# Kernel optimization log

Hardware: AMD Instinct MI355X
Metric: run time of the kernel (lower is better)

Reference implementation:

```python
import jax, jax.numpy as jnp
import numpy as np
import math

D = 2048          # embedding_size
H = 16            # nheads
HD = D // H       # head_dim
S = 2048          # seq_len
B = 2
# SwiGLU hidden per source: int(2*(4*D)/3) rounded up to multiple of 256
FF = 256 * ((int(2 * (4 * D) / 3) + 255) // 256)  # 5632
EPS = 1e-6


def pe_row(seq_len, d_model):
    # PositionalEncoding buffer, but forward uses only pe[:, seq_len-1]
    pos = float(seq_len - 1)
    div = jnp.exp(jnp.arange(0, d_model, 2, dtype=jnp.float32) * (-math.log(10000.0) / d_model))
    row = jnp.zeros((d_model,), jnp.float32)
    row = row.at[0::2].set(jnp.sin(pos * div))
    row = row.at[1::2].set(jnp.cos(pos * div))
    return row  # [D]


def rmsnorm(x, g, eps=EPS):
    xf = x.astype(jnp.float32)
    n = xf * jax.lax.rsqrt(jnp.mean(xf * xf, axis=-1, keepdims=True) + eps)
    return g * n.astype(x.dtype)


def setup_inputs() -> dict:
    key = jax.random.key(0)
    ks = jax.random.split(key, 16)
    sd = 0.02
    x = jax.random.normal(ks[0], (B, S, D), jnp.float32)
    mask = jnp.triu(jnp.ones((S, S), jnp.int32), k=1)[None, None]  # [1,1,S,S], 1 = masked
    return {
        'x': x,
        'mask': mask,
        'qkv_w': jax.random.normal(ks[1], (3 * D, D), jnp.float32) * sd,
        'qkv_b': jnp.zeros((3 * D,), jnp.float32),
        'fc_w': jax.random.normal(ks[2], (D, D), jnp.float32) * sd,
        'fc_b': jnp.zeros((D,), jnp.float32),
        'w1': jax.random.normal(ks[3], (FF, D), jnp.float32) * sd,
        'b1': jnp.zeros((FF,), jnp.float32),
        'w2': jax.random.normal(ks[4], (FF, D), jnp.float32) * sd,
        'b2': jnp.zeros((FF,), jnp.float32),
        'w3': jax.random.normal(ks[5], (D, FF), jnp.float32) * sd,
        'b3': jnp.zeros((D,), jnp.float32),
        'g_attn': jnp.ones((D,), jnp.float32),
        'g_ff': jnp.ones((D,), jnp.float32),
    }


def _block(x, mask, qkv_w, qkv_b, fc_w, fc_b, w1, b1, w2, b2, w3, b3, g_attn, g_ff):
    b, s, _ = x.shape
    # attention sublayer (pre-norm)
    h_in = rmsnorm(x, g_attn)
    qkv = h_in @ qkv_w.T + qkv_b
    xq, xk, xv = jnp.split(qkv, 3, axis=-1)
    pe = pe_row(s, D)  # single row added everywhere (faithful to source)
    xq = xq + pe
    xk = xk + pe
    q = xq.reshape(b, s, H, HD).transpose(0, 2, 1, 3)
    k = xk.reshape(b, s, H, HD).transpose(0, 2, 1, 3)
    v = xv.reshape(b, s, H, HD).transpose(0, 2, 1, 3)
    scores = jnp.einsum('bhqd,bhkd->bhqk', q, k) / math.sqrt(HD)
    scores = jnp.where(mask == 1, jnp.float32(-1e9), scores)
    attn = jax.nn.softmax(scores, axis=-1)
    out = jnp.einsum('bhqk,bhkd->bhqd', attn, v)
    out = out.transpose(0, 2, 1, 3).reshape(b, s, D)
    attn_out = out @ fc_w.T + fc_b
    h = x + attn_out
    # SwiGLU FFN sublayer (pre-norm)
    f_in = rmsnorm(h, g_ff)
    gate = jax.nn.silu(f_in @ w1.T + b1) * (f_in @ w2.T + b2)
    return h + gate @ w3.T + b3


def reference(x, mask, qkv_w, qkv_b, fc_w, fc_b, w1, b1, w2, b2, w3, b3, g_attn, g_ff):
    return _block(x, mask, qkv_w, qkv_b, fc_w, fc_b, w1, b1, w2, b2, w3, b3, g_attn, g_ff)
```

## Files before the change

kernel.cpp:

```cpp
#include <hip/hip_runtime.h>
#include <math.h>


typedef __attribute__((ext_vector_type(8))) short bf16x8;
typedef __attribute__((ext_vector_type(4))) short bf16x4;
typedef __attribute__((ext_vector_type(4))) float f32x4;

#define DEVI __device__ __forceinline__

DEVI unsigned short f2bf(float f) {
  unsigned u = __builtin_bit_cast(unsigned, f);
  u += 0x7FFFu + ((u >> 16) & 1u);
  return (unsigned short)(u >> 16);
}
DEVI float bf2f(unsigned short h) {
  unsigned u = ((unsigned)h) << 16;
  return __builtin_bit_cast(float, u);
}

#define GLL16(g, l) __builtin_amdgcn_global_load_lds( \
    (const __attribute__((address_space(1))) unsigned int*)(const void*)(g), \
    (__attribute__((address_space(3))) unsigned int*)(void*)(l), 16, 0, 0)

__global__ __launch_bounds__(256) void wconv_k(const float* __restrict__ src,
                                               unsigned short* __restrict__ dst,
                                               long n8) {
  long t = (long)blockIdx.x * 256 + threadIdx.x;
  if (t >= n8) return;
  const f32x4* s = (const f32x4*)(src + t * 8);
  f32x4 a = s[0], b = s[1];
  bf16x8 o;
#pragma unroll
  for (int j = 0; j < 4; ++j) {
    o[j]     = (short)f2bf(a[j]);
    o[4 + j] = (short)f2bf(b[j]);
  }
  *(bf16x8*)(dst + t * 8) = o;
}

__global__ void pe_k(float* __restrict__ pe) {
  int c = blockIdx.x * 256 + threadIdx.x;
  if (c >= 2048) return;
  int i2 = c & ~1;
  float div = __expf(-(float)i2 * (9.210340371976184f / 2048.0f));
  float ang = 2047.0f * div;
  pe[c] = (c & 1) ? cosf(ang) : sinf(ang);
}

__global__ __launch_bounds__(256) void rmsnorm_k(const float* __restrict__ x,
                                                 const float* __restrict__ g,
                                                 unsigned short* __restrict__ out) {
  long row = blockIdx.x;
  const float* xr = x + row * 2048;
  int tid = threadIdx.x;
  f32x4 v0 = *(const f32x4*)&xr[tid * 8];
  f32x4 v1 = *(const f32x4*)&xr[tid * 8 + 4];
  float ss = 0.f;
#pragma unroll
  for (int j = 0; j < 4; ++j) ss += v0[j] * v0[j] + v1[j] * v1[j];
#pragma unroll
  for (int m = 1; m < 64; m <<= 1) ss += __shfl_xor(ss, m, 64);
  __shared__ float red[4];
  int lane = tid & 63, wv = tid >> 6;
  if (lane == 0) red[wv] = ss;
  __syncthreads();
  float tot = red[0] + red[1] + red[2] + red[3];
  float rn = rsqrtf(tot * (1.0f / 2048.0f) + 1e-6f);
  const float* gr = g + tid * 8;
  bf16x8 o;
#pragma unroll
  for (int j = 0; j < 4; ++j) {
    o[j]     = (short)f2bf(v0[j] * rn * gr[j]);
    o[4 + j] = (short)f2bf(v1[j] * rn * gr[4 + j]);
  }
  *(bf16x8*)&out[row * 2048 + tid * 8] = o;
}

template <int EPI>
__global__ __launch_bounds__(512, 1) void gemm256(const unsigned short* __restrict__ A,
                                                  const unsigned short* __restrict__ W,
                                                  const float* __restrict__ bias,
                                                  const float* __restrict__ resid,
                                                  void* __restrict__ outv,
                                                  int M, int N, int K, int nbx) {
  __shared__ __align__(16) unsigned short Ab[3][256 * 64];
  __shared__ __align__(16) unsigned short Bb[3][128 * 64];
  const int tid  = threadIdx.x;
  const int lane = tid & 63;
  const int wv   = tid >> 6;
  const int wm   = wv >> 1;
  const int wn   = wv & 1;
  const int l15  = lane & 15;
  const int lg   = lane >> 4;
  const int cpx = gridDim.x >> 3;
  const int wg  = (blockIdx.x & 7) * cpx + (blockIdx.x >> 3);
  const long tm = (long)(wg / nbx) * 256;
  const long tn = (long)(wg % nbx) * 128;

  const int srow = wv * 8 + (lane >> 3);
  const int scol = (((lane & 7) ^ (lane >> 3)) << 3);
  const unsigned short* gA = A + (tm + srow) * (long)K + scol;
  const unsigned short* gB = W + (tn + srow) * (long)K + scol;

  const int KT = K >> 6;

#define STGA(buf, kt, g) GLL16(gA + ((long)(g) * 64) * K + ((long)(kt) << 6), \
                               &Ab[buf][(g) * 4096 + wv * 512])
#define STGB(buf, kt, g) GLL16(gB + ((long)(g) * 64) * K + ((long)(kt) << 6), \
                               &Bb[buf][(g) * 4096 + wv * 512])

  f32x4 acc[4][4] = {};

  STGA(0, 0, 0); STGA(0, 0, 1); STGA(0, 0, 2); STGA(0, 0, 3);
  STGB(0, 0, 0); STGB(0, 0, 1);
  STGA(1, 1, 0); STGA(1, 1, 1); STGA(1, 1, 2); STGA(1, 1, 3);
  STGB(1, 1, 0); STGB(1, 1, 1);
  asm volatile("s_waitcnt vmcnt(6)" ::: "memory");
  __builtin_amdgcn_s_barrier();

  int ct = 0;
  for (int t = 0; t < KT; ++t) {
    const int pt = (ct >= 1) ? (ct - 1) : 2;
    const bool pre = (t + 2) < KT;
    const unsigned short* At = &Ab[ct][0];
    const unsigned short* Bt = &Bb[ct][0];
#pragma unroll
    for (int kk = 0; kk < 2; ++kk) {
      bf16x8 af[4], bfv[4];
#pragma unroll
      for (int m = 0; m < 4; ++m)
        af[m] = *(const bf16x8*)&At[((wm * 64 + m * 16 + l15) * 8 +
                                     ((kk * 4 + lg) ^ (l15 & 7))) * 8];
#pragma unroll
      for (int n = 0; n < 4; ++n)
        bfv[n] = *(const bf16x8*)&Bt[((wn * 64 + n * 16 + l15) * 8 +
                                      ((kk * 4 + lg) ^ (l15 & 7))) * 8];
      if (pre) {
        if (kk == 0) { STGA(pt, t + 2, 0); STGA(pt, t + 2, 1); STGA(pt, t + 2, 2); }
        else         { STGA(pt, t + 2, 3); STGB(pt, t + 2, 0); STGB(pt, t + 2, 1); }
      }
      __builtin_amdgcn_s_barrier();
      __builtin_amdgcn_s_setprio(1);
#pragma unroll
      for (int m = 0; m < 4; ++m)
#pragma unroll
        for (int n = 0; n < 4; ++n)
          acc[m][n] = __builtin_amdgcn_mfma_f32_16x16x32_bf16(af[m], bfv[n], acc[m][n], 0, 0, 0);
      __builtin_amdgcn_s_setprio(0);
      if (kk == 0) {
        __builtin_amdgcn_s_barrier();
      } else {
        if (t + 2 < KT)      asm volatile("s_waitcnt vmcnt(6)" ::: "memory");
        else if (t + 1 < KT) asm volatile("s_waitcnt vmcnt(0)" ::: "memory");
        __builtin_amdgcn_s_barrier();
      }
    }
    ct = (ct + 1 >= 3) ? 0 : (ct + 1);
  }
#undef STGA
#undef STGB
  __builtin_amdgcn_sched_barrier(0);

  const long row0 = tm + wm * 64 + (lg << 2);
  const long col0 = tn + wn * 64;
#pragma unroll
  for (int n = 0; n < 4; ++n) {
    const long col = col0 + n * 16 + l15;
    const float bv = bias[col];
#pragma unroll
    for (int m = 0; m < 4; ++m) {
      const long rw = row0 + m * 16;
#pragma unroll
      for (int j = 0; j < 4; ++j) {
        const float v = acc[m][n][j] + bv;
        if (EPI == 0) {
          ((unsigned short*)outv)[(rw + j) * (long)N + col] = f2bf(v);
        } else {
          float* of = (float*)outv;
          const long i = (rw + j) * (long)N + col;
          of[i] = resid[i] + v;
        }
      }
    }
  }
}

__global__ __launch_bounds__(256) void krepack_k(const unsigned short* __restrict__ qkv,
                                                 const float* __restrict__ pe,
                                                 unsigned short* __restrict__ kpe) {
  long t = (long)blockIdx.x * 256 + threadIdx.x;
  long idx = t * 8;
  long row = idx >> 11;
  int cd  = (int)(idx & 2047);
  int h = cd >> 7, d = cd & 127;
  long b = row >> 11, s = row & 2047;
  bf16x8 v = *(const bf16x8*)&qkv[row * 6144 + 2048 + cd];
  const float* per = &pe[cd];
#pragma unroll
  for (int j = 0; j < 8; ++j)
    v[j] = (short)f2bf(bf2f((unsigned short)v[j]) + per[j]);
  *(bf16x8*)&kpe[(((b * 16 + h)) * 2048 + s) * 128 + d] = v;
}

__global__ __launch_bounds__(256) void vtrans_k(const unsigned short* __restrict__ qkv,
                                                unsigned short* __restrict__ Vt) {
  const int s0 = blockIdx.x * 64;
  const int d0 = blockIdx.y * 64;
  const int bh = blockIdx.z;
  const long b = bh >> 4;
  const int h = bh & 15;
  __shared__ unsigned short tile[64][76];
  const int t = threadIdx.x;
#pragma unroll
  for (int half = 0; half < 2; ++half) {
    int c = t + half * 256;
    int r = c >> 3;
    int cc = (c & 7) * 8;
    bf16x8 v = *(const bf16x8*)&qkv[(b * 2048 + s0 + r) * 6144 + 4096 + h * 128 + d0 + cc];
#pragma unroll
    for (int j = 0; j < 8; ++j) tile[cc + j][r] = (unsigned short)v[j];
  }
  __syncthreads();
#pragma unroll
  for (int half = 0; half < 2; ++half) {
    int c = t + half * 256;
    int dr = c >> 3;
    int sc = (c & 7) * 8;
    bf16x4 lo = *(const bf16x4*)&tile[dr][sc];
    bf16x4 hi = *(const bf16x4*)&tile[dr][sc + 4];
    bf16x8 v;
#pragma unroll
    for (int j = 0; j < 4; ++j) { v[j] = lo[j]; v[4 + j] = hi[j]; }
    *(bf16x8*)&Vt[((long)bh * 128 + d0 + dr) * 2048 + s0 + sc] = v;
  }
}

__global__ __launch_bounds__(256, 2) void fattn_k(const unsigned short* __restrict__ QKV,
                                                  const float* __restrict__ pe,
                                                  const unsigned short* __restrict__ Kp,
                                                  const unsigned short* __restrict__ Vt,
                                                  unsigned short* __restrict__ O) {
  const int lin = blockIdx.x;
  const int chunk = lin & 7;
  const int idx = lin >> 3;
  const int bh = chunk * 4 + (idx >> 4);
  const int i16 = idx & 15;
  const int qb = (i16 & 1) ? ((i16 - 1) >> 1) : (15 - (i16 >> 1));
  const long b = bh >> 4;
  const int h = bh & 15;
  const int q0 = qb * 128;
  const int tid = threadIdx.x, lane = tid & 63, wv = tid >> 6;
  const int l15 = lane & 15, lg = lane >> 4;
  const int qw = q0 + wv * 32;

  __shared__ __align__(16) unsigned short Kl[2][8192];
  __shared__ __align__(16) unsigned short Vl[2][8192];
  __shared__ __align__(16) unsigned short Plds[4][32][40];

  const float scale = 0.08838834764831845f;
  const unsigned short* Qb = QKV + (b * 2048 + qw) * 6144 + h * 128;
  bf16x8 qf[2][4];
#pragma unroll
  for (int r = 0; r < 2; ++r)
#pragma unroll
    for (int kc = 0; kc < 4; ++kc) {
      bf16x8 v = *(const bf16x8*)&Qb[(r * 16 + l15) * 6144 + kc * 32 + lg * 8];
      const float* per = &pe[h * 128 + kc * 32 + lg * 8];
#pragma unroll
      for (int j = 0; j < 8; ++j)
        v[j] = (short)f2bf((bf2f((unsigned short)v[j]) + per[j]) * scale);
      qf[r][kc] = v;
    }

  const unsigned short* Kg = Kp + (long)bh * 2048 * 128;
  const unsigned short* Vg = Vt + (long)bh * 128 * 2048;

  auto stage = [&](int buf, int key0) {
#pragma unroll
    for (int ld = 0; ld < 4; ++ld) {
      int sr = wv * 16 + ld * 4 + (lane >> 4);
      int sc = ((lane & 15) << 3) ^ ((sr & 7) << 3);
      GLL16(Kg + (long)(key0 + sr) * 128 + sc, &Kl[buf][wv * 2048 + ld * 512]);
      int dr = wv * 32 + ld * 8 + (lane >> 3);
      int dc = ((lane & 7) << 3) ^ ((dr & 7) << 3);
      GLL16(Vg + (long)dr * 2048 + key0 + dc, &Vl[buf][wv * 2048 + ld * 512]);
    }
  };

  f32x4 o[2][8] = {};
  float mr[2][4], sdn[2][4];
#pragma unroll
  for (int r = 0; r < 2; ++r)
#pragma unroll
    for (int j = 0; j < 4; ++j) { mr[r][j] = -1e30f; sdn[r][j] = 0.f; }

  const int nkt = (q0 >> 6) + 2;
  stage(0, 0);
  __syncthreads();
  int cur = 0;
  for (int kt = 0; kt < nkt; ++kt) {
    const int key0 = kt << 6;
    if (kt + 1 < nkt) stage(cur ^ 1, key0 + 64);
    if (key0 <= qw + 31) {
      f32x4 s[2][4] = {};
      __builtin_amdgcn_s_setprio(1);
#pragma unroll
      for (int ks = 0; ks < 4; ++ks) {
        bf16x8 kf[4];
#pragma unroll
        for (int kc = 0; kc < 4; ++kc)
          kf[kc] = *(const bf16x8*)&Kl[cur][(ks * 16 + l15) * 128 +
                                           ((kc * 32 + lg * 8) ^ ((l15 & 7) << 3))];
#pragma unroll
        for (int r = 0; r < 2; ++r)
#pragma unroll
          for (int kc = 0; kc < 4; ++kc)
            s[r][ks] = __builtin_amdgcn_mfma_f32_16x16x32_bf16(qf[r][kc], kf[kc], s[r][ks], 0, 0, 0);
      }
      __builtin_amdgcn_s_setprio(0);
      const bool maskt = (key0 + 63 > qw);
      float pm[2][4];
#pragma unroll
      for (int r = 0; r < 2; ++r)
#pragma unroll
        for (int j = 0; j < 4; ++j) pm[r][j] = -1e30f;
#pragma unroll
      for (int r = 0; r < 2; ++r)
#pragma unroll
        for (int ks = 0; ks < 4; ++ks)
#pragma unroll
          for (int j = 0; j < 4; ++j) {
            float v = s[r][ks][j];
            if (maskt) {
              int qrow = qw + r * 16 + lg * 4 + j;
              int key  = key0 + ks * 16 + l15;
              v = (key <= qrow) ? v : -1e30f;
              s[r][ks][j] = v;
            }
            pm[r][j] = fmaxf(pm[r][j], v);
          }
#pragma unroll
      for (int msk = 1; msk < 16; msk <<= 1)
#pragma unroll
        for (int r = 0; r < 2; ++r)
#pragma unroll
          for (int j = 0; j < 4; ++j) pm[r][j] = fmaxf(pm[r][j], __shfl_xor(pm[r][j], msk, 64));
      bool grow = false;
#pragma unroll
      for (int r = 0; r < 2; ++r)
#pragma unroll
        for (int j = 0; j < 4; ++j) grow = grow || (pm[r][j] > mr[r][j] + 8.0f);
      if (__any(grow)) {
#pragma unroll
        for (int r = 0; r < 2; ++r)
#pragma unroll
          for (int j = 0; j < 4; ++j) {
            float mn = fmaxf(mr[r][j], pm[r][j]);
            float corr = __expf(mr[r][j] - mn);
            mr[r][j] = mn;
            sdn[r][j] *= corr;
#pragma unroll
            for (int nf = 0; nf < 8; ++nf) o[r][nf][j] *= corr;
          }
      }
      float ps[2][4];
#pragma unroll
      for (int r = 0; r < 2; ++r)
#pragma unroll
        for (int j = 0; j < 4; ++j) ps[r][j] = 0.f;
#pragma unroll
      for (int r = 0; r < 2; ++r)
#pragma unroll
        for (int ks = 0; ks < 4; ++ks)
#pragma unroll
          for (int j = 0; j < 4; ++j) {
            float e = __expf(s[r][ks][j] - mr[r][j]);
            s[r][ks][j] = e;
            ps[r][j] += e;
          }
#pragma unroll
      for (int msk = 1; msk < 16; msk <<= 1)
#pragma unroll
        for (int r = 0; r < 2; ++r)
#pragma unroll
          for (int j = 0; j < 4; ++j) ps[r][j] += __shfl_xor(ps[r][j], msk, 64);
#pragma unroll
      for (int r = 0; r < 2; ++r)
#pragma unroll
        for (int j = 0; j < 4; ++j) sdn[r][j] += ps[r][j];
#pragma unroll
      for (int hk = 0; hk < 2; ++hk) {
#pragma unroll
        for (int r = 0; r < 2; ++r)
#pragma unroll
          for (int ks2 = 0; ks2 < 2; ++ks2)
#pragma unroll
            for (int j = 0; j < 4; ++j)
              Plds[wv][r * 16 + lg * 4 + j][ks2 * 16 + l15] = f2bf(s[r][hk * 2 + ks2][j]);
        bf16x8 pf[2];
#pragma unroll
        for (int r = 0; r < 2; ++r) {
          bf16x4 lo = *(const bf16x4*)&Plds[wv][r * 16 + l15][lg * 8];
          bf16x4 hi = *(const bf16x4*)&Plds[wv][r * 16 + l15][lg * 8 + 4];
          bf16x8 p;
#pragma unroll
          for (int j = 0; j < 4; ++j) { p[j] = lo[j]; p[4 + j] = hi[j]; }
          pf[r] = p;
        }
        __builtin_amdgcn_s_setprio(1);
#pragma unroll
        for (int nf = 0; nf < 8; ++nf) {
          bf16x8 vf = *(const bf16x8*)&Vl[cur][(nf * 16 + l15) * 64 +
                                              ((hk * 32 + lg * 8) ^ ((l15 & 7) << 3))];
#pragma unroll
          for (int r = 0; r < 2; ++r)
            o[r][nf] = __builtin_amdgcn_mfma_f32_16x16x32_bf16(pf[r], vf, o[r][nf], 0, 0, 0);
        }
        __builtin_amdgcn_s_setprio(0);
      }
    }
    __syncthreads();
    cur ^= 1;
  }
  unsigned short* Ob = O + (b * 2048 + qw) * 2048 + h * 128;
#pragma unroll
  for (int r = 0; r < 2; ++r)
#pragma unroll
    for (int j = 0; j < 4; ++j) {
      float inv = 1.0f / sdn[r][j];
#pragma unroll
      for (int nf = 0; nf < 8; ++nf)
        Ob[(long)(r * 16 + lg * 4 + j) * 2048 + nf * 16 + l15] = f2bf(o[r][nf][j] * inv);
    }
}

__global__ __launch_bounds__(256) void gate_k(const unsigned short* __restrict__ a1,
                                              const unsigned short* __restrict__ a2,
                                              unsigned short* __restrict__ g) {
  long idx = ((long)blockIdx.x * 256 + threadIdx.x) * 8;
  bf16x8 x1 = *(const bf16x8*)&a1[idx];
  bf16x8 x2 = *(const bf16x8*)&a2[idx];
  bf16x8 r;
#pragma unroll
  for (int j = 0; j < 8; ++j) {
    float f1 = bf2f((unsigned short)x1[j]);
    float f2v = bf2f((unsigned short)x2[j]);
    float sg = f1 / (1.0f + __expf(-f1));
    r[j] = (short)f2bf(sg * f2v);
  }
  *(bf16x8*)&g[idx] = r;
}

extern "C" void kernel_launch(void* const* d_in, const int* in_sizes, int n_in,
                              void* d_out, int out_size, void* d_ws, size_t ws_size,
                              hipStream_t stream) {
  (void)in_sizes; (void)n_in; (void)out_size; (void)ws_size;
  const float* x    = (const float*)d_in[0];
  const float* qkvw = (const float*)d_in[2];
  const float* qkvb = (const float*)d_in[3];
  const float* fcw  = (const float*)d_in[4];
  const float* fcb  = (const float*)d_in[5];
  const float* w1   = (const float*)d_in[6];
  const float* b1   = (const float*)d_in[7];
  const float* w2   = (const float*)d_in[8];
  const float* b2   = (const float*)d_in[9];
  const float* w3   = (const float*)d_in[10];
  const float* b3   = (const float*)d_in[11];
  const float* ga   = (const float*)d_in[12];
  const float* gf   = (const float*)d_in[13];

  char* ws = (char*)d_ws;
  size_t off = 0;
  auto alloc = [&](size_t bytes) -> char* {
    char* p = ws + off;
    off = (off + bytes + 255) & ~(size_t)255;
    return p;
  };
  unsigned short* wqkv  = (unsigned short*)alloc(6144L * 2048 * 2);
  unsigned short* wfc   = (unsigned short*)alloc(2048L * 2048 * 2);
  unsigned short* w1b   = (unsigned short*)alloc(5632L * 2048 * 2);
  unsigned short* w2b   = (unsigned short*)alloc(5632L * 2048 * 2);
  unsigned short* w3b   = (unsigned short*)alloc(2048L * 5632 * 2);
  float*          pe    = (float*)alloc(2048 * 4);
  unsigned short* hin   = (unsigned short*)alloc(4096L * 2048 * 2);
  unsigned short* qkv   = (unsigned short*)alloc(4096L * 6144 * 2);
  unsigned short* kpe   = (unsigned short*)alloc(4096L * 2048 * 2);
  unsigned short* Vt    = (unsigned short*)alloc(4096L * 2048 * 2);
  unsigned short* attnb = (unsigned short*)alloc(4096L * 2048 * 2);
  float* h = (float*)d_out;

  wconv_k<<<6144, 256, 0, stream>>>(qkvw, wqkv, 6144L * 2048 / 8);
  wconv_k<<<2048, 256, 0, stream>>>(fcw,  wfc,  2048L * 2048 / 8);
  wconv_k<<<5632, 256, 0, stream>>>(w1,   w1b,  5632L * 2048 / 8);
  wconv_k<<<5632, 256, 0, stream>>>(w2,   w2b,  5632L * 2048 / 8);
  wconv_k<<<5632, 256, 0, stream>>>(w3,   w3b,  2048L * 5632 / 8);
  pe_k<<<8, 256, 0, stream>>>(pe);

  rmsnorm_k<<<4096, 256, 0, stream>>>(x, ga, hin);
  gemm256<0><<<768, 512, 0, stream>>>(hin, wqkv, qkvb, nullptr, qkv, 4096, 6144, 2048, 48);
  krepack_k<<<4096, 256, 0, stream>>>(qkv, pe, kpe);
  vtrans_k<<<dim3(32, 2, 32), 256, 0, stream>>>(qkv, Vt);
  fattn_k<<<dim3(512), 256, 0, stream>>>(qkv, pe, kpe, Vt, attnb);
  gemm256<1><<<256, 512, 0, stream>>>(attnb, wfc, fcb, x, h, 4096, 2048, 2048, 16);

  rmsnorm_k<<<4096, 256, 0, stream>>>(h, gf, hin);
  unsigned short* a1 = qkv;
  unsigned short* a2 = kpe;
  gemm256<0><<<704, 512, 0, stream>>>(hin, w1b, b1, nullptr, a1, 4096, 5632, 2048, 44);
  gemm256<0><<<704, 512, 0, stream>>>(hin, w2b, b2, nullptr, a2, 4096, 5632, 2048, 44);
  gate_k<<<11264, 256, 0, stream>>>(a1, a2, a1);
  gemm256<1><<<256, 512, 0, stream>>>(a1, w3b, b3, h, d_out, 4096, 2048, 5632, 16);
}
```

Measured before the change: 772.8 us.

## Switch GEMM to double-buffered split-K-half LDS layout and split attention launch

Result: slower. 885.6 us (+14.6%).

```diff
diff --git a/kernel.cpp b/kernel.cpp
--- a/kernel.cpp
+++ b/kernel.cpp
@@ -77,14 +77,14 @@
 }
 
 template <int EPI>
-__global__ __launch_bounds__(512, 1) void gemm256(const unsigned short* __restrict__ A,
-                                                  const unsigned short* __restrict__ W,
-                                                  const float* __restrict__ bias,
-                                                  const float* __restrict__ resid,
-                                                  void* __restrict__ outv,
-                                                  int M, int N, int K, int nbx) {
-  __shared__ __align__(16) unsigned short Ab[3][256 * 64];
-  __shared__ __align__(16) unsigned short Bb[3][128 * 64];
+__global__ __launch_bounds__(512, 1) void gemm2(const unsigned short* __restrict__ A,
+                                                const unsigned short* __restrict__ W,
+                                                const float* __restrict__ bias,
+                                                const float* __restrict__ resid,
+                                                void* __restrict__ outv,
+                                                int M, int N, int K, int nbx) {
+  __shared__ __align__(16) unsigned short AL[2][16384];
+  __shared__ __align__(16) unsigned short BL[2][8192];
   const int tid  = threadIdx.x;
   const int lane = tid & 63;
   const int wv   = tid >> 6;
@@ -97,48 +97,42 @@
   const long tm = (long)(wg / nbx) * 256;
   const long tn = (long)(wg % nbx) * 128;
 
-  const int srow = wv * 8 + (lane >> 3);
-  const int scol = (((lane & 7) ^ (lane >> 3)) << 3);
-  const unsigned short* gA = A + (tm + srow) * (long)K + scol;
-  const unsigned short* gB = W + (tn + srow) * (long)K + scol;
-
+  const int q   = lane >> 2;
+  const int s4  = lane & 3;
+  const int srl = wv * 16 + q;
+  const int scol = ((s4 ^ ((q >> 1) & 3)) << 3);
+  const unsigned short* pA = A + (long)(tm + srl) * K + scol;
+  const unsigned short* pB = W + (long)(tn + srl) * K + scol;
+
+#define SGA(buf, kt, ks) do {                                                       \
+    GLL16(pA + ((long)(kt) << 6) + ((ks) << 5), &AL[buf][(ks)*8192 + (wv*16)*32]);  \
+    GLL16(pA + 128L*K + ((long)(kt) << 6) + ((ks) << 5),                            \
+          &AL[buf][(ks)*8192 + (128 + wv*16)*32]);                                  \
+  } while (0)
+#define SGB(buf, kt, ks) GLL16(pB + ((long)(kt) << 6) + ((ks) << 5),                \
+                               &BL[buf][(ks)*4096 + (wv*16)*32])
+
+  f32x4 acc[4][4] = {};
   const int KT = K >> 6;
 
-#define STGA(buf, kt, g) GLL16(gA + ((long)(g) * 64) * K + ((long)(kt) << 6), \
-                               &Ab[buf][(g) * 4096 + wv * 512])
-#define STGB(buf, kt, g) GLL16(gB + ((long)(g) * 64) * K + ((long)(kt) << 6), \
-                               &Bb[buf][(g) * 4096 + wv * 512])
-
-  f32x4 acc[4][4] = {};
-
-  STGA(0, 0, 0); STGA(0, 0, 1); STGA(0, 0, 2); STGA(0, 0, 3);
-  STGB(0, 0, 0); STGB(0, 0, 1);
-  STGA(1, 1, 0); STGA(1, 1, 1); STGA(1, 1, 2); STGA(1, 1, 3);
-  STGB(1, 1, 0); STGB(1, 1, 1);
-  asm volatile("s_waitcnt vmcnt(6)" ::: "memory");
+  SGA(0, 0, 0); SGB(0, 0, 0); SGA(0, 0, 1); SGB(0, 0, 1);
+  asm volatile("s_waitcnt vmcnt(0)" ::: "memory");
   __builtin_amdgcn_s_barrier();
 
-  int ct = 0;
+  const int sw = (lg ^ ((l15 >> 1) & 3)) << 3;
   for (int t = 0; t < KT; ++t) {
-    const int pt = (ct >= 1) ? (ct - 1) : 2;
-    const bool pre = (t + 2) < KT;
-    const unsigned short* At = &Ab[ct][0];
-    const unsigned short* Bt = &Bb[ct][0];
-#pragma unroll
-    for (int kk = 0; kk < 2; ++kk) {
+    const int b = t & 1, nb = b ^ 1;
+    const bool stg = (t + 1) < KT;
+#pragma unroll
+    for (int ks = 0; ks < 2; ++ks) {
       bf16x8 af[4], bfv[4];
 #pragma unroll
       for (int m = 0; m < 4; ++m)
-        af[m] = *(const bf16x8*)&At[((wm * 64 + m * 16 + l15) * 8 +
-                                     ((kk * 4 + lg) ^ (l15 & 7))) * 8];
+        af[m] = *(const bf16x8*)&AL[b][ks * 8192 + (wm * 64 + m * 16 + l15) * 32 + sw];
 #pragma unroll
       for (int n = 0; n < 4; ++n)
-        bfv[n] = *(const bf16x8*)&Bt[((wn * 64 + n * 16 + l15) * 8 +
-                                      ((kk * 4 + lg) ^ (l15 & 7))) * 8];
-      if (pre) {
-        if (kk == 0) { STGA(pt, t + 2, 0); STGA(pt, t + 2, 1); STGA(pt, t + 2, 2); }
-        else         { STGA(pt, t + 2, 3); STGB(pt, t + 2, 0); STGB(pt, t + 2, 1); }
-      }
+        bfv[n] = *(const bf16x8*)&BL[b][ks * 4096 + (wn * 64 + n * 16 + l15) * 32 + sw];
+      if (stg) { SGA(nb, t + 1, ks); SGB(nb, t + 1, ks); }
       __builtin_amdgcn_s_barrier();
       __builtin_amdgcn_s_setprio(1);
 #pragma unroll
@@ -147,18 +141,18 @@
         for (int n = 0; n < 4; ++n)
           acc[m][n] = __builtin_amdgcn_mfma_f32_16x16x32_bf16(af[m], bfv[n], acc[m][n], 0, 0, 0);
       __builtin_amdgcn_s_setprio(0);
-      if (kk == 0) {
+      if (ks == 0) {
+        if (stg) asm volatile("s_waitcnt vmcnt(3)" ::: "memory");
+        else     asm volatile("s_waitcnt vmcnt(0)" ::: "memory");
         __builtin_amdgcn_s_barrier();
-      } else {
-        if (t + 2 < KT)      asm volatile("s_waitcnt vmcnt(6)" ::: "memory");
-        else if (t + 1 < KT) asm volatile("s_waitcnt vmcnt(0)" ::: "memory");
+      } else if (stg) {
+        asm volatile("s_waitcnt vmcnt(3)" ::: "memory");
         __builtin_amdgcn_s_barrier();
       }
     }
-    ct = (ct + 1 >= 3) ? 0 : (ct + 1);
-  }
-#undef STGA
-#undef STGB
+  }
+#undef SGA
+#undef SGB
   __builtin_amdgcn_sched_barrier(0);
 
   const long row0 = tm + wm * 64 + (lg << 2);
@@ -239,13 +233,14 @@
                                                   const float* __restrict__ pe,
                                                   const unsigned short* __restrict__ Kp,
                                                   const unsigned short* __restrict__ Vt,
-                                                  unsigned short* __restrict__ O) {
+                                                  unsigned short* __restrict__ O,
+                                                  int qbase) {
   const int lin = blockIdx.x;
   const int chunk = lin & 7;
   const int idx = lin >> 3;
-  const int bh = chunk * 4 + (idx >> 4);
-  const int i16 = idx & 15;
-  const int qb = (i16 & 1) ? ((i16 - 1) >> 1) : (15 - (i16 >> 1));
+  const int bh = chunk * 4 + (idx >> 3);
+  const int qsub = idx & 7;
+  const int qb = qbase + ((qsub & 1) ? (qsub >> 1) : (7 - (qsub >> 1)));
   const long b = bh >> 4;
   const int h = bh & 15;
   const int q0 = qb * 128;
@@ -497,17 +492,18 @@
   pe_k<<<8, 256, 0, stream>>>(pe);
 
   rmsnorm_k<<<4096, 256, 0, stream>>>(x, ga, hin);
-  gemm256<0><<<768, 512, 0, stream>>>(hin, wqkv, qkvb, nullptr, qkv, 4096, 6144, 2048, 48);
+  gemm2<0><<<768, 512, 0, stream>>>(hin, wqkv, qkvb, nullptr, qkv, 4096, 6144, 2048, 48);
   krepack_k<<<4096, 256, 0, stream>>>(qkv, pe, kpe);
   vtrans_k<<<dim3(32, 2, 32), 256, 0, stream>>>(qkv, Vt);
-  fattn_k<<<dim3(512), 256, 0, stream>>>(qkv, pe, kpe, Vt, attnb);
-  gemm256<1><<<256, 512, 0, stream>>>(attnb, wfc, fcb, x, h, 4096, 2048, 2048, 16);
+  fattn_k<<<dim3(256), 256, 0, stream>>>(qkv, pe, kpe, Vt, attnb, 8);
+  fattn_k<<<dim3(256), 256, 0, stream>>>(qkv, pe, kpe, Vt, attnb, 0);
+  gemm2<1><<<256, 512, 0, stream>>>(attnb, wfc, fcb, x, h, 4096, 2048, 2048, 16);
 
   rmsnorm_k<<<4096, 256, 0, stream>>>(h, gf, hin);
   unsigned short* a1 = qkv;
   unsigned short* a2 = kpe;
-  gemm256<0><<<704, 512, 0, stream>>>(hin, w1b, b1, nullptr, a1, 4096, 5632, 2048, 44);
-  gemm256<0><<<704, 512, 0, stream>>>(hin, w2b, b2, nullptr, a2, 4096, 5632, 2048, 44);
+  gemm2<0><<<704, 512, 0, stream>>>(hin, w1b, b1, nullptr, a1, 4096, 5632, 2048, 44);
+  gemm2<0><<<704, 512, 0, stream>>>(hin, w2b, b2, nullptr, a2, 4096, 5632, 2048, 44);
   gate_k<<<11264, 256, 0, stream>>>(a1, a2, a1);
-  gemm256<1><<<256, 512, 0, stream>>>(a1, w3b, b3, h, d_out, 4096, 2048, 5632, 16);
-}
+  gemm2<1><<<256, 512, 0, stream>>>(a1, w3b, b3, h, d_out, 4096, 2048, 5632, 16);
+}
```
